# Kernel tuning notes

Measured on AMD Instinct MI355X. Metric: run time of the kernel, lower is better.

Reference implementation:

```python
import jax, jax.numpy as jnp
import numpy as np

N_GENE, N_DIS = 100_000, 50_000   # node counts per node type
D = 128                            # hidden_channels (= input dim, required by skipsum)
E = 800_000                        # edges per edge type
L = 2                              # num_layers
EPS = 1e-12                        # torch F.normalize eps


def setup_inputs() -> dict:
    key = jax.random.key(0)
    ks = jax.random.split(key, 9)
    s = 1.0 / np.sqrt(D)
    return {
        "x_gene": jax.random.normal(ks[0], (N_GENE, D), jnp.float32),
        "x_disease": jax.random.normal(ks[1], (N_DIS, D), jnp.float32),
        # per (layer, edge_type) SAGEConv weights: lin_l (neighbors), lin_r (root), bias
        # edge_type 0: gene->disease, edge_type 1: disease->gene
        "Wl": jax.random.normal(ks[2], (L, 2, D, D), jnp.float32) * s,
        "Wr": jax.random.normal(ks[3], (L, 2, D, D), jnp.float32) * s,
        "b": jax.random.normal(ks[4], (L, 2, D), jnp.float32) * 0.01,
        "src_g2d": jax.random.randint(ks[5], (E,), 0, N_GENE, dtype=jnp.int32),
        "dst_g2d": jax.random.randint(ks[6], (E,), 0, N_DIS, dtype=jnp.int32),
        "src_d2g": jax.random.randint(ks[7], (E,), 0, N_DIS, dtype=jnp.int32),
        "dst_d2g": jax.random.randint(ks[8], (E,), 0, N_GENE, dtype=jnp.int32),
    }


def _sage(x_src, x_dst, src, dst, Wl, Wr, b, n_dst):
    # SAGEConv with aggr='mean': lin_l(mean_{j in N(i)} x_j) + lin_r(x_i) + bias
    msg = jnp.take(x_src, src, axis=0)                                   # [E, D] gather
    summed = jax.ops.segment_sum(msg, dst, num_segments=n_dst)           # [n_dst, D]
    cnt = jax.ops.segment_sum(jnp.ones_like(src, dtype=x_src.dtype), dst,
                              num_segments=n_dst)                        # [n_dst]
    mean = summed / jnp.maximum(cnt, 1.0)[:, None]                       # isolated nodes -> 0
    return mean @ Wl.T + x_dst @ Wr.T + b


def _l2norm(x):
    n = jnp.linalg.norm(x, axis=-1, keepdims=True)
    return x / jnp.maximum(n, EPS)


def reference(x_gene, x_disease, Wl, Wr, b, src_g2d, dst_g2d, src_d2g, dst_d2g):
    xg, xd = x_gene, x_disease
    for i in range(L):
        # to_hetero: one conv per edge type; macro_aggregation='sum' across edge types
        # (each dst type here receives exactly one edge type)
        hd = _sage(xg, xd, src_g2d, dst_g2d, Wl[i, 0], Wr[i, 0], b[i, 0], N_DIS)
        hg = _sage(xd, xg, src_d2g, dst_d2g, Wl[i, 1], Wr[i, 1], b[i, 1], N_GENE)
        if i < L - 1:  # hidden layers get the activation
            hg, hd = jax.nn.relu(hg), jax.nn.relu(hd)
        # L2_norm=True -> normalize every layer
        hg, hd = _l2norm(hg), _l2norm(hd)
        # skipsum
        xg, xd = hg + xg, hd + xd
    return xg, xd
```

## Files before the change

### kernel.cpp

```cpp
#include <hip/hip_runtime.h>
#include <math.h>

#define NG 100000
#define ND 50000
#define NTOT 150000
#define DIM 128
#define NE 800000
#define EPSN 1e-12f

#define RPB 128
#define NBT_D3 391
#define NBT_G3 782

#define NBK 586
#define SCB 128
#define EPB 12500

typedef __bf16 bf16x8 __attribute__((ext_vector_type(8)));
typedef float f32x4 __attribute__((ext_vector_type(4)));
typedef unsigned int uint32;

__device__ __forceinline__ ushort rne_bf16(float f) {
  uint32 u = __builtin_bit_cast(uint32, f);
  u += 0x7fffu + ((u >> 16) & 1u);
  return (ushort)(u >> 16);
}

__device__ __forceinline__ void gload_lds16(const void* g, void* l) {
  __builtin_amdgcn_global_load_lds((const __attribute__((address_space(1))) void*)g,
                                   (__attribute__((address_space(3))) void*)l, 16, 0, 0);
}


__global__ void zero_ints(int* __restrict__ p, int n) {
  int i = blockIdx.x * 256 + threadIdx.x;
  if (i < n) p[i] = 0;
}

__global__ void bucket_count(const int* __restrict__ dst_g2d, const int* __restrict__ dst_d2g,
                             int* __restrict__ bcnt) {
  __shared__ int h[NBK];
  for (int j = threadIdx.x; j < NBK; j += 256) h[j] = 0;
  __syncthreads();
  int stride = gridDim.x * 256;
  for (int i = blockIdx.x * 256 + threadIdx.x; i < 2 * NE; i += stride) {
    int d = (i < NE) ? dst_g2d[i] : ND + dst_d2g[i - NE];
    atomicAdd(&h[d >> 8], 1);
  }
  __syncthreads();
  for (int j = threadIdx.x; j < NBK; j += 256)
    if (h[j]) atomicAdd(&bcnt[j], h[j]);
}

__global__ void bucket_scan(const int* __restrict__ bcnt, int* __restrict__ bbase,
                            int* __restrict__ bcur) {
  __shared__ int s[1024];
  int t = threadIdx.x;
  s[t] = (t < NBK) ? bcnt[t] : 0;
  __syncthreads();
  for (int off = 1; off < 1024; off <<= 1) {
    int v = (t >= off) ? s[t - off] : 0;
    __syncthreads();
    s[t] += v;
    __syncthreads();
  }
  if (t < NBK) {
    int e = (t > 0) ? s[t - 1] : 0;
    bbase[t] = e;
    bcur[t] = e;
  }
  if (t == 0) bbase[NBK] = 2 * NE;
}

__global__ void bucket_scatter(const int* __restrict__ src_g2d, const int* __restrict__ dst_g2d,
                               const int* __restrict__ src_d2g, const int* __restrict__ dst_d2g,
                               int* __restrict__ bcur, int2* __restrict__ pairs) {
  __shared__ int h[NBK];
  __shared__ int base[NBK];
  int e0 = blockIdx.x * EPB;
  int e1 = e0 + EPB;
  if (e1 > 2 * NE) e1 = 2 * NE;
  for (int j = threadIdx.x; j < NBK; j += 256) h[j] = 0;
  __syncthreads();
  for (int i = e0 + threadIdx.x; i < e1; i += 256) {
    int d = (i < NE) ? dst_g2d[i] : ND + dst_d2g[i - NE];
    atomicAdd(&h[d >> 8], 1);
  }
  __syncthreads();
  for (int j = threadIdx.x; j < NBK; j += 256) {
    int c = h[j];
    base[j] = c ? atomicAdd(&bcur[j], c) : 0;
    h[j] = 0;
  }
  __syncthreads();
  for (int i = e0 + threadIdx.x; i < e1; i += 256) {
    int d, s;
    if (i < NE) {
      d = dst_g2d[i];
      s = src_g2d[i];
    } else {
      d = ND + dst_d2g[i - NE];
      s = src_d2g[i - NE];
    }
    int bkt = d >> 8;
    int p = base[bkt] + atomicAdd(&h[bkt], 1);
    pairs[p] = make_int2(d, s);
  }
}

__global__ void bucket_to_csr(const int* __restrict__ bbase, const int2* __restrict__ pairs,
                              int* __restrict__ off, int* __restrict__ csr) {
  __shared__ int cnt[256];
  __shared__ int ss[256];
  int b = blockIdx.x, t = threadIdx.x;
  int n0 = b << 8;
  int s0 = bbase[b], s1 = bbase[b + 1];
  cnt[t] = 0;
  __syncthreads();
  for (int i = s0 + t; i < s1; i += 256) atomicAdd(&cnt[pairs[i].x - n0], 1);
  __syncthreads();
  int x = cnt[t];
  ss[t] = x;
  __syncthreads();
  for (int o = 1; o < 256; o <<= 1) {
    int y = (t >= o) ? ss[t - o] : 0;
    __syncthreads();
    ss[t] += y;
    __syncthreads();
  }
  int abs0 = s0 + ss[t] - x;
  int node = n0 + t;
  if (node < NTOT) off[node] = abs0;
  if (node == NTOT - 1) off[NTOT] = 2 * NE;
  __syncthreads();
  cnt[t] = abs0;
  __syncthreads();
  for (int i = s0 + t; i < s1; i += 256) {
    int2 e = pairs[i];
    int p = atomicAdd(&cnt[e.x - n0], 1);
    csr[p] = e.y;
  }
}


__global__ void to_bf16_all(const float* __restrict__ xg, const float* __restrict__ xd,
                            ushort* __restrict__ yg, ushort* __restrict__ yd) {
  int i = blockIdx.x * 256 + threadIdx.x;
  if (i >= NTOT * 16) return;
  const float* x;
  ushort* y;
  int j;
  if (i < NG * 16) {
    x = xg; y = yg; j = i;
  } else {
    x = xd; y = yd; j = i - NG * 16;
  }
  const float4* px = (const float4*)x;
  float4 a = px[2 * j], b = px[2 * j + 1];
  float v[8] = {a.x, a.y, a.z, a.w, b.x, b.y, b.z, b.w};
  uint32 u[4];
#pragma unroll
  for (int k = 0; k < 4; k++)
    u[k] = (uint32)rne_bf16(v[2 * k]) | ((uint32)rne_bf16(v[2 * k + 1]) << 16);
  ((int4*)y)[j] = make_int4((int)u[0], (int)u[1], (int)u[2], (int)u[3]);
}


__global__ void split_w(const float* __restrict__ Wl, const float* __restrict__ Wr,
                        ushort* __restrict__ WlH, ushort* __restrict__ WlL,
                        ushort* __restrict__ WrH, ushort* __restrict__ WrL) {
  int i = blockIdx.x * 256 + threadIdx.x;
  if (i >= 4 * 128 * 128) return;
  {
    float a = Wl[i];
    uint32 u = __builtin_bit_cast(uint32, a);
    float hf = __builtin_bit_cast(float, u & 0xffff0000u);
    WlH[i] = (ushort)(u >> 16);
    WlL[i] = (ushort)(__builtin_bit_cast(uint32, a - hf) >> 16);
  }
  {
    float a = Wr[i];
    uint32 u = __builtin_bit_cast(uint32, a);
    float hf = __builtin_bit_cast(float, u & 0xffff0000u);
    WrH[i] = (ushort)(u >> 16);
    WrL[i] = (ushort)(__builtin_bit_cast(uint32, a - hf) >> 16);
  }
}


__device__ __forceinline__ void acc8(float* a, int4 u) {
  uint32 w;
  w = (uint32)u.x;
  a[0] += __builtin_bit_cast(float, w << 16);
  a[1] += __builtin_bit_cast(float, w & 0xffff0000u);
  w = (uint32)u.y;
  a[2] += __builtin_bit_cast(float, w << 16);
  a[3] += __builtin_bit_cast(float, w & 0xffff0000u);
  w = (uint32)u.z;
  a[4] += __builtin_bit_cast(float, w << 16);
  a[5] += __builtin_bit_cast(float, w & 0xffff0000u);
  w = (uint32)u.w;
  a[6] += __builtin_bit_cast(float, w << 16);
  a[7] += __builtin_bit_cast(float, w & 0xffff0000u);
}

__global__ void agg_comb(const ushort* __restrict__ xg_bf, const ushort* __restrict__ xd_bf,
                         const int* __restrict__ off, const int* __restrict__ csr,
                         ushort* __restrict__ agg_bf) {
  int node = (blockIdx.x * 256 + threadIdx.x) >> 4;
  if (node >= NTOT) return;
  int l16 = threadIdx.x & 15;
  const int4* xs = (const int4*)((node < ND) ? xg_bf : xd_bf);
  int e0 = off[node], e1 = off[node + 1];
  float a[8] = {0.f, 0.f, 0.f, 0.f, 0.f, 0.f, 0.f, 0.f};
  int e = e0;
  for (; e + 7 < e1; e += 8) {
    int s[8];
#pragma unroll
    for (int j = 0; j < 8; j++) s[j] = csr[e + j];
    int4 v[8];
#pragma unroll
    for (int j = 0; j < 8; j++) v[j] = xs[(size_t)s[j] * 16 + l16];
#pragma unroll
    for (int j = 0; j < 8; j++) acc8(a, v[j]);
  }
  for (; e + 3 < e1; e += 4) {
    int s0 = csr[e], s1 = csr[e + 1], s2 = csr[e + 2], s3 = csr[e + 3];
    int4 v0 = xs[(size_t)s0 * 16 + l16];
    int4 v1 = xs[(size_t)s1 * 16 + l16];
    int4 v2 = xs[(size_t)s2 * 16 + l16];
    int4 v3 = xs[(size_t)s3 * 16 + l16];
    acc8(a, v0);
    acc8(a, v1);
    acc8(a, v2);
    acc8(a, v3);
  }
  for (; e + 1 < e1; e += 2) {
    int s0 = csr[e], s1 = csr[e + 1];
    int4 v0 = xs[(size_t)s0 * 16 + l16];
    int4 v1 = xs[(size_t)s1 * 16 + l16];
    acc8(a, v0);
    acc8(a, v1);
  }
  if (e < e1) acc8(a, xs[(size_t)csr[e] * 16 + l16]);
  int deg = e1 - e0;
  float inv = (deg > 0) ? 1.f / (float)deg : 0.f;
  uint32 u[4];
#pragma unroll
  for (int j = 0; j < 4; j++)
    u[j] = (uint32)rne_bf16(a[2 * j] * inv) | ((uint32)rne_bf16(a[2 * j + 1] * inv) << 16);
  *(int4*)&agg_bf[(size_t)node * DIM + l16 * 8] =
      make_int4((int)u[0], (int)u[1], (int)u[2], (int)u[3]);
}


__device__ __forceinline__ void split8v(float4 f0, float4 f1, bf16x8& hi, bf16x8& lo) {
  float v[8] = {f0.x, f0.y, f0.z, f0.w, f1.x, f1.y, f1.z, f1.w};
  uint32 hw[4], lw[4];
#pragma unroll
  for (int j = 0; j < 4; j++) {
    uint32 u0 = __builtin_bit_cast(uint32, v[2 * j]);
    uint32 u1 = __builtin_bit_cast(uint32, v[2 * j + 1]);
    float hf0 = __builtin_bit_cast(float, u0 & 0xffff0000u);
    float hf1 = __builtin_bit_cast(float, u1 & 0xffff0000u);
    uint32 l0 = __builtin_bit_cast(uint32, v[2 * j] - hf0) >> 16;
    uint32 l1 = __builtin_bit_cast(uint32, v[2 * j + 1] - hf1) >> 16;
    hw[j] = (u0 >> 16) | ((u1 >> 16) << 16);
    lw[j] = l0 | (l1 << 16);
  }
  hi = __builtin_bit_cast(bf16x8, make_int4((int)hw[0], (int)hw[1], (int)hw[2], (int)hw[3]));
  lo = __builtin_bit_cast(bf16x8, make_int4((int)lw[0], (int)lw[1], (int)lw[2], (int)lw[3]));
}

__launch_bounds__(256, 2)
__global__ void sage_dual(const ushort* __restrict__ agg_bf, const float* __restrict__ xd,
                          const float* __restrict__ xg, const ushort* __restrict__ WlH,
                          const ushort* __restrict__ WlL, const ushort* __restrict__ WrH,
                          const ushort* __restrict__ WrL, const float* __restrict__ bias_all,
                          float* __restrict__ outd, float* __restrict__ outg,
                          ushort* __restrict__ xbf_d, ushort* __restrict__ xbf_g, int layer,
                          int relu, int write_bf) {
  __shared__ __align__(16) char smem[65536];

  int b = blockIdx.x;
  const float* X;
  float* O;
  ushort* OBF;
  int n, set, r0g, cbase;
  if (b < NBT_D3) {
    X = xd; O = outd; OBF = xbf_d; n = ND; set = layer * 2; r0g = b * RPB; cbase = 0;
  } else {
    X = xg; O = outg; OBF = xbf_g; n = NG; set = layer * 2 + 1;
    r0g = (b - NBT_D3) * RPB; cbase = ND;
  }
  const ushort* Wplanes[4] = {WlH + set * 16384, WlL + set * 16384, WrH + set * 16384,
                              WrL + set * 16384};
  const float* bias = bias_all + set * 128;

  int tid = threadIdx.x;
  int wave = tid >> 6, lane = tid & 63;
  int m = lane & 15, q = lane >> 4;
  int rb = r0g + wave * 32;

  int rp[2];
#pragma unroll
  for (int mt = 0; mt < 2; mt++) {
    int r = rb + mt * 16 + m;
    rp[mt] = (r >= n) ? (n - 1) : r;
  }

  auto stageW_async = [&](const ushort* Ph, const ushort* Pl) {
#pragma unroll
    for (int i = 0; i < 16; i++) {
      int cc = wave * 16 + i;
      int dstb = cc * 1024 + lane * 16;
      int p = cc >> 5;
      int pb = dstb & 32767;
      int srcb = pb ^ (((pb >> 8) & 7) << 4);
      const char* src = (const char*)(p ? Pl : Ph) + srcb;
      gload_lds16(src, smem + cc * 1024);
    }
  };

  stageW_async(Wplanes[0], Wplanes[1]);
  int4 aV[4][2];
#pragma unroll
  for (int ks = 0; ks < 4; ks++)
#pragma unroll
    for (int mt = 0; mt < 2; mt++)
      aV[ks][mt] = *(const int4*)&agg_bf[(size_t)(cbase + rp[mt]) * DIM + ks * 32 + q * 8];
  __syncthreads();

  f32x4 acc[2][8];
#pragma unroll
  for (int mt = 0; mt < 2; mt++)
#pragma unroll
    for (int nt = 0; nt < 8; nt++) acc[mt][nt] = (f32x4)0.f;

#pragma unroll
  for (int ks = 0; ks < 4; ks++) {
    int kb = ks * 64 + q * 16;
#pragma unroll
    for (int nt = 0; nt < 8; nt++) {
      int nn = nt * 16 + m;
      int wb = (nn * 256 + kb) ^ ((nn & 7) << 4);
      bf16x8 bh = *(const bf16x8*)(smem + wb);
      bf16x8 bl = *(const bf16x8*)(smem + 32768 + wb);
#pragma unroll
      for (int mt = 0; mt < 2; mt++) {
        bf16x8 a = __builtin_bit_cast(bf16x8, aV[ks][mt]);
        acc[mt][nt] = __builtin_amdgcn_mfma_f32_16x16x32_bf16(a, bh, acc[mt][nt], 0, 0, 0);
        acc[mt][nt] = __builtin_amdgcn_mfma_f32_16x16x32_bf16(a, bl, acc[mt][nt], 0, 0, 0);
      }
    }
  }

  float4 xV[2][2];
#pragma unroll
  for (int mt = 0; mt < 2; mt++) {
#pragma unroll
    for (int h = 0; h < 2; h++)
      xV[mt][h] = *(const float4*)&X[(size_t)rp[mt] * DIM + q * 8 + h * 4];
  }
  __syncthreads();
  stageW_async(Wplanes[2], Wplanes[3]);
  __syncthreads();

#pragma unroll
  for (int ks = 0; ks < 4; ks++) {
    int kb = ks * 64 + q * 16;
    bf16x8 ah[2], al[2];
#pragma unroll
    for (int mt = 0; mt < 2; mt++) split8v(xV[mt][0], xV[mt][1], ah[mt], al[mt]);
    if (ks < 3) {
#pragma unroll
      for (int mt = 0; mt < 2; mt++) {
#pragma unroll
        for (int h = 0; h < 2; h++)
          xV[mt][h] = *(const float4*)&X[(size_t)rp[mt] * DIM + (ks + 1) * 32 + q * 8 + h * 4];
      }
    }
#pragma unroll
    for (int nt = 0; nt < 8; nt++) {
      int nn = nt * 16 + m;
      int wb = (nn * 256 + kb) ^ ((nn & 7) << 4);
      bf16x8 bh = *(const bf16x8*)(smem + wb);
      bf16x8 bl = *(const bf16x8*)(smem + 32768 + wb);
#pragma unroll
      for (int mt = 0; mt < 2; mt++) {
        acc[mt][nt] = __builtin_amdgcn_mfma_f32_16x16x32_bf16(ah[mt], bh, acc[mt][nt], 0, 0, 0);
        acc[mt][nt] = __builtin_amdgcn_mfma_f32_16x16x32_bf16(ah[mt], bl, acc[mt][nt], 0, 0, 0);
        acc[mt][nt] = __builtin_amdgcn_mfma_f32_16x16x32_bf16(al[mt], bh, acc[mt][nt], 0, 0, 0);
      }
    }
  }
  __syncthreads();

  float bb[8];
#pragma unroll
  for (int nt = 0; nt < 8; nt++) bb[nt] = bias[nt * 16 + m];

  const int S = 132;
  float* wbuf = (float*)smem + wave * (16 * S);

  int half = lane >> 5;
  int c4 = (lane & 31) * 4;

#pragma unroll
  for (int mt = 0; mt < 2; mt++) {
#pragma unroll
    for (int reg = 0; reg < 4; reg++) {
      float h[8];
      float ss = 0.f;
#pragma unroll
      for (int nt = 0; nt < 8; nt++) {
        float v = acc[mt][nt][reg] + bb[nt];
        if (relu) v = fmaxf(v, 0.f);
        h[nt] = v;
        ss += v * v;
      }
      ss += __shfl_xor(ss, 1);
      ss += __shfl_xor(ss, 2);
      ss += __shfl_xor(ss, 4);
      ss += __shfl_xor(ss, 8);
      float inv = 1.f / fmaxf(sqrtf(ss), EPSN);
      int rrel = q * 4 + reg;
#pragma unroll
      for (int nt = 0; nt < 8; nt++) wbuf[rrel * S + nt * 16 + m] = h[nt] * inv;
    }
#pragma unroll
    for (int i = 0; i < 8; i++) {
      int rrel = i * 2 + half;
      int R = rb + mt * 16 + rrel;
      if (R < n) {
        f32x4 hv = *(const f32x4*)&wbuf[rrel * S + c4];
        float4 xr = *(const float4*)&X[(size_t)R * DIM + c4];
        float4 o;
        o.x = hv[0] + xr.x;
        o.y = hv[1] + xr.y;
        o.z = hv[2] + xr.z;
        o.w = hv[3] + xr.w;
        *(float4*)&O[(size_t)R * DIM + c4] = o;
        if (write_bf) {
          int2 pk = make_int2((int)((uint32)rne_bf16(o.x) | ((uint32)rne_bf16(o.y) << 16)),
                              (int)((uint32)rne_bf16(o.z) | ((uint32)rne_bf16(o.w) << 16)));
          *(int2*)&OBF[(size_t)R * DIM + c4] = pk;
        }
      }
    }
  }
}


extern "C" void kernel_launch(void* const* d_in, const int* in_sizes, int n_in,
                              void* d_out, int out_size, void* d_ws, size_t ws_size,
                              hipStream_t stream) {
  const float* xg0 = (const float*)d_in[0];
  const float* xd0 = (const float*)d_in[1];
  const float* Wl = (const float*)d_in[2];
  const float* Wr = (const float*)d_in[3];
  const float* bs = (const float*)d_in[4];
  const int* src_g2d = (const int*)d_in[5];
  const int* dst_g2d = (const int*)d_in[6];
  const int* src_d2g = (const int*)d_in[7];
  const int* dst_d2g = (const int*)d_in[8];

  float* out_xg = (float*)d_out;
  float* out_xd = (float*)d_out + (size_t)NG * DIM;

  char* p = (char*)d_ws;
  auto alloc = [&](size_t bytes) -> char* {
    char* q = p;
    p += (bytes + 255) & ~(size_t)255;
    return q;
  };
  int* off = (int*)alloc((NTOT + 1) * 4);
  int* csr = (int*)alloc((size_t)2 * NE * 4);
  int* bcnt = (int*)alloc(NBK * 4);
  int* bbase = (int*)alloc((NBK + 1) * 4);
  int* bcur = (int*)alloc(NBK * 4);
  char* big = alloc((size_t)NTOT * DIM * 2);
  int2* pairs = (int2*)big;
  ushort* agg_bf = (ushort*)big;
  ushort* xg_bf = (ushort*)alloc((size_t)NG * DIM * 2);
  ushort* xd_bf = (ushort*)alloc((size_t)ND * DIM * 2);
  ushort* WlH = (ushort*)alloc((size_t)4 * 128 * 128 * 2);
  ushort* WlL = (ushort*)alloc((size_t)4 * 128 * 128 * 2);
  ushort* WrH = (ushort*)alloc((size_t)4 * 128 * 128 * 2);
  ushort* WrL = (ushort*)alloc((size_t)4 * 128 * 128 * 2);

  const int TB = 256;

  split_w<<<256, TB, 0, stream>>>(Wl, Wr, WlH, WlL, WrH, WrL);
  to_bf16_all<<<(NTOT * 16 + TB - 1) / TB, TB, 0, stream>>>(xg0, xd0, xg_bf, xd_bf);

  zero_ints<<<(NBK + TB - 1) / TB, TB, 0, stream>>>(bcnt, NBK);
  bucket_count<<<256, TB, 0, stream>>>(dst_g2d, dst_d2g, bcnt);
  bucket_scan<<<1, 1024, 0, stream>>>(bcnt, bbase, bcur);
  bucket_scatter<<<SCB, TB, 0, stream>>>(src_g2d, dst_g2d, src_d2g, dst_d2g, bcur, pairs);
  bucket_to_csr<<<NBK, TB, 0, stream>>>(bbase, pairs, off, csr);

  int aggBlocks = (NTOT * 16 + TB - 1) / TB;
  int sageBlocks = NBT_D3 + NBT_G3;

  agg_comb<<<aggBlocks, TB, 0, stream>>>(xg_bf, xd_bf, off, csr, agg_bf);
  sage_dual<<<sageBlocks, TB, 0, stream>>>(agg_bf, xd0, xg0, WlH, WlL, WrH, WrL, bs, out_xd,
                                           out_xg, xd_bf, xg_bf, 0, 1, 1);

  agg_comb<<<aggBlocks, TB, 0, stream>>>(xg_bf, xd_bf, off, csr, agg_bf);
  sage_dual<<<sageBlocks, TB, 0, stream>>>(agg_bf, out_xd, out_xg, WlH, WlL, WrH, WrL, bs,
                                           out_xd, out_xg, xd_bf, xg_bf, 1, 0, 0);
}
```

Measured before the change: 468.5 us.

## Replace bucket-sort CSR build with per-node atomic count, scan, and scatter

Replaces the two-level bucket sort (bucket count, bucket scatter of pairs, per-bucket local CSR) with a direct CSR build: global atomic per-node degree counts, a two-level prefix scan, then an atomic-cursor scatter of source indices. This drops the intermediate int2 pairs buffer and one pass over it. The cost is 1.6M global atomics spread over 150K counters, twice over, instead of LDS atomics. Neighbor order within a node becomes nondeterministic, which can change floating-point summation order in aggregation.

```diff
diff --git a/kernel.cpp b/kernel.cpp
--- a/kernel.cpp
+++ b/kernel.cpp
@@ -13,8 +13,6 @@
 #define NBT_G3 782
 
 #define NBK 586
-#define SCB 128
-#define EPB 12500
 
 typedef __bf16 bf16x8 __attribute__((ext_vector_type(8)));
 typedef float f32x4 __attribute__((ext_vector_type(4)));
@@ -37,26 +35,36 @@
   if (i < n) p[i] = 0;
 }
 
-__global__ void bucket_count(const int* __restrict__ dst_g2d, const int* __restrict__ dst_d2g,
-                             int* __restrict__ bcnt) {
-  __shared__ int h[NBK];
-  for (int j = threadIdx.x; j < NBK; j += 256) h[j] = 0;
-  __syncthreads();
-  int stride = gridDim.x * 256;
-  for (int i = blockIdx.x * 256 + threadIdx.x; i < 2 * NE; i += stride) {
-    int d = (i < NE) ? dst_g2d[i] : ND + dst_d2g[i - NE];
-    atomicAdd(&h[d >> 8], 1);
-  }
-  __syncthreads();
-  for (int j = threadIdx.x; j < NBK; j += 256)
-    if (h[j]) atomicAdd(&bcnt[j], h[j]);
-}
-
-__global__ void bucket_scan(const int* __restrict__ bcnt, int* __restrict__ bbase,
-                            int* __restrict__ bcur) {
+__global__ void count_edges(const int* __restrict__ dst_g2d, const int* __restrict__ dst_d2g,
+                            int* __restrict__ cnt) {
+  int i = blockIdx.x * 256 + threadIdx.x;
+  if (i >= 2 * NE) return;
+  int d = (i < NE) ? dst_g2d[i] : ND + dst_d2g[i - NE];
+  atomicAdd(&cnt[d], 1);
+}
+
+__global__ void scan_local(const int* __restrict__ cnt, int* __restrict__ loc,
+                           int* __restrict__ bsum) {
+  __shared__ int ss[256];
+  int b = blockIdx.x, t = threadIdx.x;
+  int idx = b * 256 + t;
+  int c = (idx < NTOT) ? cnt[idx] : 0;
+  ss[t] = c;
+  __syncthreads();
+  for (int o = 1; o < 256; o <<= 1) {
+    int y = (t >= o) ? ss[t - o] : 0;
+    __syncthreads();
+    ss[t] += y;
+    __syncthreads();
+  }
+  if (idx < NTOT) loc[idx] = ss[t] - c;
+  if (t == 255) bsum[b] = ss[255];
+}
+
+__global__ void scan_blocks(const int* __restrict__ bsum, int* __restrict__ bbase) {
   __shared__ int s[1024];
   int t = threadIdx.x;
-  s[t] = (t < NBK) ? bcnt[t] : 0;
+  s[t] = (t < NBK) ? bsum[t] : 0;
   __syncthreads();
   for (int off = 1; off < 1024; off <<= 1) {
     int v = (t >= off) ? s[t - off] : 0;
@@ -64,82 +72,35 @@
     s[t] += v;
     __syncthreads();
   }
-  if (t < NBK) {
-    int e = (t > 0) ? s[t - 1] : 0;
-    bbase[t] = e;
-    bcur[t] = e;
-  }
-  if (t == 0) bbase[NBK] = 2 * NE;
-}
-
-__global__ void bucket_scatter(const int* __restrict__ src_g2d, const int* __restrict__ dst_g2d,
-                               const int* __restrict__ src_d2g, const int* __restrict__ dst_d2g,
-                               int* __restrict__ bcur, int2* __restrict__ pairs) {
-  __shared__ int h[NBK];
-  __shared__ int base[NBK];
-  int e0 = blockIdx.x * EPB;
-  int e1 = e0 + EPB;
-  if (e1 > 2 * NE) e1 = 2 * NE;
-  for (int j = threadIdx.x; j < NBK; j += 256) h[j] = 0;
-  __syncthreads();
-  for (int i = e0 + threadIdx.x; i < e1; i += 256) {
-    int d = (i < NE) ? dst_g2d[i] : ND + dst_d2g[i - NE];
-    atomicAdd(&h[d >> 8], 1);
-  }
-  __syncthreads();
-  for (int j = threadIdx.x; j < NBK; j += 256) {
-    int c = h[j];
-    base[j] = c ? atomicAdd(&bcur[j], c) : 0;
-    h[j] = 0;
-  }
-  __syncthreads();
-  for (int i = e0 + threadIdx.x; i < e1; i += 256) {
-    int d, s;
-    if (i < NE) {
-      d = dst_g2d[i];
-      s = src_g2d[i];
-    } else {
-      d = ND + dst_d2g[i - NE];
-      s = src_d2g[i - NE];
-    }
-    int bkt = d >> 8;
-    int p = base[bkt] + atomicAdd(&h[bkt], 1);
-    pairs[p] = make_int2(d, s);
-  }
-}
-
-__global__ void bucket_to_csr(const int* __restrict__ bbase, const int2* __restrict__ pairs,
-                              int* __restrict__ off, int* __restrict__ csr) {
-  __shared__ int cnt[256];
-  __shared__ int ss[256];
-  int b = blockIdx.x, t = threadIdx.x;
-  int n0 = b << 8;
-  int s0 = bbase[b], s1 = bbase[b + 1];
-  cnt[t] = 0;
-  __syncthreads();
-  for (int i = s0 + t; i < s1; i += 256) atomicAdd(&cnt[pairs[i].x - n0], 1);
-  __syncthreads();
-  int x = cnt[t];
-  ss[t] = x;
-  __syncthreads();
-  for (int o = 1; o < 256; o <<= 1) {
-    int y = (t >= o) ? ss[t - o] : 0;
-    __syncthreads();
-    ss[t] += y;
-    __syncthreads();
-  }
-  int abs0 = s0 + ss[t] - x;
-  int node = n0 + t;
-  if (node < NTOT) off[node] = abs0;
-  if (node == NTOT - 1) off[NTOT] = 2 * NE;
-  __syncthreads();
-  cnt[t] = abs0;
-  __syncthreads();
-  for (int i = s0 + t; i < s1; i += 256) {
-    int2 e = pairs[i];
-    int p = atomicAdd(&cnt[e.x - n0], 1);
-    csr[p] = e.y;
-  }
+  if (t < NBK) bbase[t] = (t > 0) ? s[t - 1] : 0;
+}
+
+__global__ void finalize_off(int* __restrict__ off, const int* __restrict__ bbase,
+                             int* __restrict__ cur) {
+  int i = blockIdx.x * 256 + threadIdx.x;
+  if (i < NTOT) {
+    int v = off[i] + bbase[i >> 8];
+    off[i] = v;
+    cur[i] = v;
+  }
+  if (i == 0) off[NTOT] = 2 * NE;
+}
+
+__global__ void scatter_edges(const int* __restrict__ src_g2d, const int* __restrict__ dst_g2d,
+                              const int* __restrict__ src_d2g, const int* __restrict__ dst_d2g,
+                              int* __restrict__ cur, int* __restrict__ csr) {
+  int i = blockIdx.x * 256 + threadIdx.x;
+  if (i >= 2 * NE) return;
+  int d, s;
+  if (i < NE) {
+    d = dst_g2d[i];
+    s = src_g2d[i];
+  } else {
+    d = ND + dst_d2g[i - NE];
+    s = src_d2g[i - NE];
+  }
+  int p = atomicAdd(&cur[d], 1);
+  csr[p] = s;
 }
 
 
@@ -476,12 +437,10 @@
   };
   int* off = (int*)alloc((NTOT + 1) * 4);
   int* csr = (int*)alloc((size_t)2 * NE * 4);
-  int* bcnt = (int*)alloc(NBK * 4);
+  int* cur = (int*)alloc(NTOT * 4);
+  int* bsum = (int*)alloc(NBK * 4);
   int* bbase = (int*)alloc((NBK + 1) * 4);
-  int* bcur = (int*)alloc(NBK * 4);
-  char* big = alloc((size_t)NTOT * DIM * 2);
-  int2* pairs = (int2*)big;
-  ushort* agg_bf = (ushort*)big;
+  ushort* agg_bf = (ushort*)alloc((size_t)NTOT * DIM * 2);
   ushort* xg_bf = (ushort*)alloc((size_t)NG * DIM * 2);
   ushort* xd_bf = (ushort*)alloc((size_t)ND * DIM * 2);
   ushort* WlH = (ushort*)alloc((size_t)4 * 128 * 128 * 2);
@@ -490,15 +449,17 @@
   ushort* WrL = (ushort*)alloc((size_t)4 * 128 * 128 * 2);
 
   const int TB = 256;
+  const int EB = (2 * NE + TB - 1) / TB;
 
   split_w<<<256, TB, 0, stream>>>(Wl, Wr, WlH, WlL, WrH, WrL);
   to_bf16_all<<<(NTOT * 16 + TB - 1) / TB, TB, 0, stream>>>(xg0, xd0, xg_bf, xd_bf);
 
-  zero_ints<<<(NBK + TB - 1) / TB, TB, 0, stream>>>(bcnt, NBK);
-  bucket_count<<<256, TB, 0, stream>>>(dst_g2d, dst_d2g, bcnt);
-  bucket_scan<<<1, 1024, 0, stream>>>(bcnt, bbase, bcur);
-  bucket_scatter<<<SCB, TB, 0, stream>>>(src_g2d, dst_g2d, src_d2g, dst_d2g, bcur, pairs);
-  bucket_to_csr<<<NBK, TB, 0, stream>>>(bbase, pairs, off, csr);
+  zero_ints<<<(NTOT + TB - 1) / TB, TB, 0, stream>>>(cur, NTOT);
+  count_edges<<<EB, TB, 0, stream>>>(dst_g2d, dst_d2g, cur);
+  scan_local<<<NBK, TB, 0, stream>>>(cur, off, bsum);
+  scan_blocks<<<1, 1024, 0, stream>>>(bsum, bbase);
+  finalize_off<<<NBK, TB, 0, stream>>>(off, bbase, cur);
+  scatter_edges<<<EB, TB, 0, stream>>>(src_g2d, dst_g2d, src_d2g, dst_d2g, cur, csr);
 
   int aggBlocks = (NTOT * 16 + TB - 1) / TB;
   int sageBlocks = NBT_D3 + NBT_G3;
```

Measured after the change: 567.9 us. 21.2% more time.
